# Optimization experiments

Measured on AMD Instinct MI355X. Metric: run time of the kernel, lower is better.

The kernel has to match this reference:

```python
import jax, jax.numpy as jnp
import numpy as np

# Conv-TasNet style TCN: 32 DepthConv1d blocks (8 in, 8 shared, 8 out-branch1, 8 out-branch2)
NUM_BLOCKS = 32
LAYER = 8
DILS = [2 ** (i % LAYER) for i in range(NUM_BLOCKS)]
C_IN, BN, H, OUT, K = 256, 128, 512, 256, 3
B, T = 4, 4000
EPS = 1e-8


def _prelu(x, a):
    return jnp.where(x >= 0, x, a * x)


def _gn(x, g, b):
    # GroupNorm(1, C): normalize over (C, T) per sample. x: [B, C, T]
    m = jnp.mean(x, axis=(1, 2), keepdims=True)
    v = jnp.var(x, axis=(1, 2), keepdims=True)
    return (x - m) * jax.lax.rsqrt(v + EPS) * g[None, :, None] + b[None, :, None]


def _dwconv(x, w, d):
    # depthwise dilated conv, same-length output. x: [B, H, T], w: [H, K]
    return jax.lax.conv_general_dilated(
        x, w[:, None, :], window_strides=(1,), padding=[(d, d)],
        rhs_dilation=(d,), dimension_numbers=('NCH', 'OIH', 'NCH'),
        feature_group_count=w.shape[0])


def _block(x, i, pw_w, pw_b, dw_w, dw_b, res_w, res_b, sk_w, sk_b,
           p1, p2, n1g, n1b, n2g, n2b):
    d = DILS[i]
    y = jnp.einsum('hc,bct->bht', pw_w[i], x) + pw_b[i][None, :, None]
    y = _gn(_prelu(y, p1[i]), n1g[i], n1b[i])
    y = _dwconv(y, dw_w[i], d) + dw_b[i][None, :, None]
    y = _gn(_prelu(y, p2[i]), n2g[i], n2b[i])
    res = jnp.einsum('ch,bht->bct', res_w[i], y) + res_b[i][None, :, None]
    skip = jnp.einsum('ch,bht->bct', sk_w[i], y) + sk_b[i][None, :, None]
    return res, skip


def setup_inputs() -> dict:
    key = jax.random.key(0)
    ks = iter(jax.random.split(key, 64))

    def rn(shape, s=0.05):
        return jax.random.normal(next(ks), shape, dtype=jnp.float32) * s

    L = NUM_BLOCKS
    return {
        'input_r': jax.random.normal(next(ks), (B, C_IN, T), dtype=jnp.float32),
        'ln1_g': jnp.ones((C_IN,), jnp.float32),
        'ln1_b': jnp.zeros((C_IN,), jnp.float32),
        'bn1_w': rn((BN, C_IN)), 'bn1_b': jnp.zeros((BN,), jnp.float32),
        'pw_w': rn((L, H, BN)), 'pw_b': jnp.zeros((L, H), jnp.float32),
        'dw_w': rn((L, H, K)), 'dw_b': jnp.zeros((L, H), jnp.float32),
        'res_w': rn((L, BN, H)), 'res_b': jnp.zeros((L, BN), jnp.float32),
        'sk_w': rn((L, BN, H)), 'sk_b': jnp.zeros((L, BN), jnp.float32),
        'p1': jnp.full((L,), 0.25, jnp.float32), 'p2': jnp.full((L,), 0.25, jnp.float32),
        'n1g': jnp.ones((L, H), jnp.float32), 'n1b': jnp.zeros((L, H), jnp.float32),
        'n2g': jnp.ones((L, H), jnp.float32), 'n2b': jnp.zeros((L, H), jnp.float32),
        'h1_p': jnp.array(0.25, jnp.float32),
        'h1_w': rn((OUT, BN)), 'h1_b': jnp.zeros((OUT,), jnp.float32),
        'h2_p': jnp.array(0.25, jnp.float32),
        'h2_w': rn((OUT, BN)), 'h2_b': jnp.zeros((OUT,), jnp.float32),
    }


def reference(input_r, ln1_g, ln1_b, bn1_w, bn1_b, pw_w, pw_b, dw_w, dw_b,
              res_w, res_b, sk_w, sk_b, p1, p2, n1g, n1b, n2g, n2b,
              h1_p, h1_w, h1_b, h2_p, h2_w, h2_b):
    bp = (pw_w, pw_b, dw_w, dw_b, res_w, res_b, sk_w, sk_b,
          p1, p2, n1g, n1b, n2g, n2b)
    out = _gn(input_r, ln1_g, ln1_b)
    out = jnp.einsum('oc,bct->bot', bn1_w, out) + bn1_b[None, :, None]
    skip_r = jnp.zeros_like(out)
    # TCN_in1: blocks 0..7
    for i in range(0, 8):
        r, s = _block(out, i, *bp)
        out = out + r
        skip_r = skip_r + s
    feature_r = out
    # shared TCN: blocks 8..15
    for i in range(8, 16):
        r, s = _block(out, i, *bp)
        out = out + r
        skip_r = skip_r + s
    o1, o2 = out, out
    sk1, sk2 = skip_r, skip_r
    # TCN_out1: blocks 16..23; TCN_out2: blocks 24..31
    for j in range(8):
        r, s = _block(o1, 16 + j, *bp)
        o1 = o1 + r
        sk1 = sk1 + s
        r, s = _block(o2, 24 + j, *bp)
        o2 = o2 + r
        sk2 = sk2 + s
    out1 = jnp.einsum('oc,bct->bot', h1_w, _prelu(sk1, h1_p)) + h1_b[None, :, None]
    out2 = jnp.einsum('oc,bct->bot', h2_w, _prelu(sk2, h2_p)) + h2_b[None, :, None]
    return out1, out2, feature_r
```

## Files before the change

### kernel.cpp

```cpp
#include <hip/hip_runtime.h>
#include <hip/hip_bf16.h>


#define T_  4000
#define TP_ 4096
#define B_  4
#define YHAL 128
#define YROW 512
#define YSST ((size_t)(TP_ + 2 * YHAL) * YROW)
#define USST ((size_t)TP_ * YROW)
#define NSUB 64
#define SLOTW (NSUB * 8)

typedef __attribute__((ext_vector_type(8))) short  s8v;
typedef __attribute__((ext_vector_type(4))) float  f32x4;
typedef __attribute__((ext_vector_type(4))) unsigned short u16x4;

__device__ __forceinline__ float bf2f(unsigned short u) {
  unsigned int i = ((unsigned int)u) << 16;
  float f; __builtin_memcpy(&f, &i, 4); return f;
}
__device__ __forceinline__ unsigned short f2bf(float f) {
  unsigned int i; __builtin_memcpy(&i, &f, 4);
  unsigned int r = i + 0x7fffu + ((i >> 16) & 1u);
  return (unsigned short)(r >> 16);
}

__device__ __forceinline__ void g2lds16(const void* g, void* l) {
  __builtin_amdgcn_global_load_lds(
      (const __attribute__((address_space(1))) unsigned int*)g,
      (__attribute__((address_space(3))) unsigned int*)l, 16, 0, 0);
}

__device__ __forceinline__ void stats_sum(const float* __restrict__ si, int b,
                                          float& u, float& q) {
  const int lane = threadIdx.x & 63;
  u = si[lane * 8 + b * 2 + 0];
  q = si[lane * 8 + b * 2 + 1];
#pragma unroll
  for (int off = 32; off > 0; off >>= 1) {
    u += __shfl_xor(u, off);
    q += __shfl_xor(q, off);
  }
}

__global__ __launch_bounds__(256) void gn_stats(const float* __restrict__ X,
                                                float* __restrict__ statsOut, int n) {
  const int b = blockIdx.y;
  const float4* xp = (const float4*)(X + (size_t)b * n);
  const int n4 = n >> 2;
  float s1 = 0.f, s2 = 0.f;
  for (int idx = blockIdx.x * 256 + threadIdx.x; idx < n4; idx += gridDim.x * 256) {
    float4 v = xp[idx];
    s1 += v.x + v.y + v.z + v.w;
    s2 += v.x * v.x + v.y * v.y + v.z * v.z + v.w * v.w;
  }
#pragma unroll
  for (int off = 32; off > 0; off >>= 1) {
    s1 += __shfl_xor(s1, off);
    s2 += __shfl_xor(s2, off);
  }
  __shared__ float red[8];
  const int lane = threadIdx.x & 63, wv = threadIdx.x >> 6;
  if (lane == 0) { red[wv] = s1; red[4 + wv] = s2; }
  __syncthreads();
  if (threadIdx.x == 0) {
    float* dst = statsOut + (size_t)(blockIdx.x & (NSUB - 1)) * 8 + b * 2;
    atomicAdd(&dst[0], red[0] + red[1] + red[2] + red[3]);
    atomicAdd(&dst[1], red[4] + red[5] + red[6] + red[7]);
  }
}

__global__ __launch_bounds__(256) void cvt_bf(const float* __restrict__ s,
                                              unsigned short* __restrict__ d, int n) {
  for (int i = blockIdx.x * 256 + threadIdx.x; i < n; i += gridDim.x * 256)
    d[i] = f2bf(s[i]);
}

__global__ __launch_bounds__(256) void fold_rs(
    const float* __restrict__ rw, const float* __restrict__ sw,
    const float* __restrict__ g2a, const float* __restrict__ b2a,
    unsigned short* __restrict__ Wg, float* __restrict__ Ucb,
    float* __restrict__ Vcb) {
  const int row = blockIdx.x;
  const int i = row >> 8, m = row & 255;
  const float* src = (m < 128) ? rw + ((size_t)i * 128 + m) * 512
                               : sw + ((size_t)i * 128 + (m - 128)) * 512;
  const float* g = g2a + (size_t)i * 512;
  const float* bb = b2a + (size_t)i * 512;
  unsigned short* dst = Wg + (size_t)row * 512;
  float u = 0.f, v = 0.f;
  for (int h = threadIdx.x; h < 512; h += 256) {
    float wgt = src[h] * g[h];
    dst[h] = f2bf(wgt);
    u += wgt; v += src[h] * bb[h];
  }
#pragma unroll
  for (int off = 32; off > 0; off >>= 1) {
    u += __shfl_xor(u, off);
    v += __shfl_xor(v, off);
  }
  __shared__ float red[8];
  const int lane = threadIdx.x & 63, wv = threadIdx.x >> 6;
  if (lane == 0) { red[wv] = u; red[4 + wv] = v; }
  __syncthreads();
  if (threadIdx.x == 0) {
    Ucb[row] = red[0] + red[1] + red[2] + red[3];
    Vcb[row] = red[4] + red[5] + red[6] + red[7];
  }
}

__global__ __launch_bounds__(256) void prelu2(const float* __restrict__ S0,
                                              const float* __restrict__ S1,
                                              unsigned short* __restrict__ D,
                                              const float* __restrict__ a0p,
                                              const float* __restrict__ a1p, int n) {
  const float a0 = a0p[0], a1 = a1p[0];
  for (int i = blockIdx.x * 256 + threadIdx.x; i < 2 * n; i += gridDim.x * 256) {
    float v = (i < n) ? S0[i] : S1[i - n];
    float a = (i < n) ? a0 : a1;
    v = v >= 0.f ? v : a * v;
    D[i] = f2bf(v);
  }
}

__global__ __launch_bounds__(256) void tin(const float* __restrict__ X,
                                           unsigned short* __restrict__ Xt,
                                           const float* __restrict__ g,
                                           const float* __restrict__ bt,
                                           const float* __restrict__ sIn, float invN) {
  const int b = blockIdx.z, c0 = blockIdx.y * 64, t0 = blockIdx.x * 64;
  __shared__ float tile[64][65];
  const int tid = threadIdx.x;
  float su, sq;
  stats_sum(sIn, b, su, sq);
  const float mean = su * invN;
  const float rs = rsqrtf(sq * invN - mean * mean + 1e-8f);
  {
    const int cl = tid >> 2, tq = (tid & 3) * 16;
    const float* Xr = X + ((size_t)b * 256 + c0 + cl) * T_;
#pragma unroll
    for (int j = 0; j < 4; ++j) {
      int tt = t0 + tq + j * 4;
      float4 v;
      if (tt + 3 < T_) v = *(const float4*)(Xr + tt);
      else {
        v.x = (tt + 0 < T_) ? Xr[tt + 0] : 0.f;
        v.y = (tt + 1 < T_) ? Xr[tt + 1] : 0.f;
        v.z = (tt + 2 < T_) ? Xr[tt + 2] : 0.f;
        v.w = (tt + 3 < T_) ? Xr[tt + 3] : 0.f;
      }
      tile[cl][tq + j * 4 + 0] = v.x; tile[cl][tq + j * 4 + 1] = v.y;
      tile[cl][tq + j * 4 + 2] = v.z; tile[cl][tq + j * 4 + 3] = v.w;
    }
  }
  __syncthreads();
  {
    const int tl = tid >> 2, cq = (tid & 3) * 16;
    const int t = t0 + tl;
    if (t < T_) {
      unsigned short* dst = Xt + ((size_t)b * TP_ + t) * 256 + c0 + cq;
      s8v u0, u1;
#pragma unroll
      for (int j = 0; j < 16; ++j) {
        int c = c0 + cq + j;
        float sc = rs * g[c];
        float oc = bt[c] - mean * sc;
        unsigned short uu = f2bf(tile[cq + j][tl] * sc + oc);
        if (j < 8) u0[j] = (short)uu; else u1[j - 8] = (short)uu;
      }
      *(s8v*)dst = u0;
      *(s8v*)(dst + 8) = u1;
    }
  }
}

struct MMP {
  const unsigned short *A0, *A1, *B0, *B1;
  const float *bias0, *bias1;
  float *O0a, *O0b, *O1a, *O1b;
  unsigned short *Obf0, *Obf1;
  const float *al0, *al1;
  float *so0, *so1;
  const float *si0, *si1;
  const float *Uc0, *Uc1, *Vc0, *Vc1, *rb0, *rb1, *sb0, *sb1;
  float* feat;
  float* dupO0; unsigned short* dupObf; float* dupO1;
  int K; float invN;
};

template <int EPI, int TN, int FLG>
__global__ __launch_bounds__(256) void mm6(MMP p) {
  constexpr bool PAIR = (FLG & 1) != 0;
  constexpr bool WF   = (FLG & 2) != 0;
  constexpr bool DUPF = (FLG & 4) != 0;
  constexpr int NJ = TN / 32;
  __shared__ unsigned short As[128 * 64];
  __shared__ unsigned short Bs[TN * 64];
  __shared__ float redw[8];
  int b = blockIdx.z; bool br2 = false;
  if constexpr (PAIR) {
    const int h = gridDim.z >> 1;
    if (b >= h) { br2 = true; b -= h; }
  }
  const int K = p.K;
  const unsigned short* A  = br2 ? p.A1 : p.A0;
  const unsigned short* Bm = br2 ? p.B1 : p.B0;
  const int m0 = blockIdx.y * 128;
  const int t0 = blockIdx.x * TN;
  const int tid = threadIdx.x;
  const int lane = tid & 63;
  const int w = tid >> 6;
  const int wm = w >> 1, wn = w & 1;
  const int lt = lane & 15, lg = lane >> 4;
  const unsigned short* Ab = A + (size_t)m0 * K;
  const unsigned short* Bb = Bm + ((size_t)b * TP_ + t0) * K;
  const int srow8 = lane >> 3;
  const int skc   = ((lane & 7) ^ (lane >> 3)) * 8;

  f32x4 acc[4][NJ];
#pragma unroll
  for (int i = 0; i < 4; ++i)
#pragma unroll
    for (int j = 0; j < NJ; ++j) acc[i][j] = (f32x4){0.f, 0.f, 0.f, 0.f};

  for (int k0 = 0; k0 < K; k0 += 64) {
#pragma unroll
    for (int c = 0; c < 4; ++c) {
      const int ch = w * 4 + c;
      g2lds16(Ab + (size_t)(ch * 8 + srow8) * K + k0 + skc, &As[ch * 512]);
    }
#pragma unroll
    for (int c = 0; c < NJ; ++c) {
      const int ch = w * NJ + c;
      g2lds16(Bb + (size_t)(ch * 8 + srow8) * K + k0 + skc, &Bs[ch * 512]);
    }
    __syncthreads();
#pragma unroll
    for (int ks = 0; ks < 2; ++ks) {
      s8v bfr[NJ];
#pragma unroll
      for (int j = 0; j < NJ; ++j) {
        const int R = wn * (TN / 2) + j * 16 + lt;
        bfr[j] = *(const s8v*)&Bs[R * 64 + (((ks * 4 + lg) ^ (R & 7)) * 8)];
      }
#pragma unroll
      for (int i = 0; i < 4; ++i) {
        const int R = wm * 64 + i * 16 + lt;
        s8v af = *(const s8v*)&As[R * 64 + (((ks * 4 + lg) ^ (R & 7)) * 8)];
#pragma unroll
        for (int j = 0; j < NJ; ++j)
          acc[i][j] = __builtin_amdgcn_mfma_f32_16x16x32_bf16(af, bfr[j], acc[i][j], 0, 0, 0);
      }
    }
    __syncthreads();
  }

  if constexpr (EPI == 0) {
    const float* bias = p.bias0;
#pragma unroll
    for (int i = 0; i < 4; ++i) {
      const int mg = m0 + wm * 64 + i * 16 + lg * 4;
      float4 bi = *(const float4*)(bias + mg);
#pragma unroll
      for (int j = 0; j < NJ; ++j) {
        const int t = t0 + wn * (TN / 2) + j * 16 + lt;
        f32x4 v = acc[i][j];
        float nv[4] = {v[0] + bi.x, v[1] + bi.y, v[2] + bi.z, v[3] + bi.w};
        *(float4*)(p.O0a + ((size_t)b * TP_ + t) * 128 + mg) =
            make_float4(nv[0], nv[1], nv[2], nv[3]);
        u16x4 pk;
#pragma unroll
        for (int r = 0; r < 4; ++r) pk[r] = f2bf(nv[r]);
        *(u16x4*)(p.Obf0 + ((size_t)b * TP_ + t) * 128 + mg) = pk;
      }
    }
  } else if constexpr (EPI == 1) {
    const float* bias = br2 ? p.bias1 : p.bias0;
    unsigned short* Obf = (br2 ? p.Obf1 : p.Obf0) + (size_t)b * YSST;
    const float aO = (br2 ? p.al1 : p.al0)[0];
    float* so = br2 ? p.so1 : p.so0;
    float s1 = 0.f, s2 = 0.f;
#pragma unroll
    for (int i = 0; i < 4; ++i) {
      const int mg = m0 + wm * 64 + i * 16 + lg * 4;
      float4 bi = *(const float4*)(bias + mg);
      float bv[4] = {bi.x, bi.y, bi.z, bi.w};
#pragma unroll
      for (int j = 0; j < NJ; ++j) {
        const int t = t0 + wn * (TN / 2) + j * 16 + lt;
        f32x4 v = acc[i][j];
        u16x4 pk;
#pragma unroll
        for (int r = 0; r < 4; ++r) {
          float f = v[r] + bv[r];
          f = f >= 0.f ? f : aO * f;
          pk[r] = f2bf(f);
        }
        *(u16x4*)(Obf + (size_t)t * YROW + mg) = pk;
        if (t < T_) {
#pragma unroll
          for (int r = 0; r < 4; ++r) { float f = bf2f(pk[r]); s1 += f; s2 += f * f; }
        }
      }
    }
#pragma unroll
    for (int off = 32; off > 0; off >>= 1) {
      s1 += __shfl_xor(s1, off);
      s2 += __shfl_xor(s2, off);
    }
    if (lane == 0) { redw[w] = s1; redw[4 + w] = s2; }
    __syncthreads();
    if (tid == 0) {
      float* dst = so + (size_t)(blockIdx.x & (NSUB - 1)) * 8 + b * 2;
      atomicAdd(&dst[0], redw[0] + redw[1] + redw[2] + redw[3]);
      atomicAdd(&dst[1], redw[4] + redw[5] + redw[6] + redw[7]);
    }
  } else if constexpr (EPI == 2) {
    float* O0 = br2 ? p.O0b : p.O0a;
    float* O1 = br2 ? p.O1b : p.O1a;
    unsigned short* Obf = br2 ? p.Obf1 : p.Obf0;
    const float* si = br2 ? p.si1 : p.si0;
    const float* Uc = br2 ? p.Uc1 : p.Uc0;
    const float* Vc = br2 ? p.Vc1 : p.Vc0;
    const float* rb = br2 ? p.rb1 : p.rb0;
    const float* sb = br2 ? p.sb1 : p.sb0;
    float su, sq;
    stats_sum(si, b, su, sq);
    const float mean = su * p.invN;
    const float rsv = rsqrtf(sq * p.invN - mean * mean + 1e-8f);
    const bool isRes = (m0 == 0);
#pragma unroll
    for (int i = 0; i < 4; ++i) {
      const int ml = wm * 64 + i * 16 + lg * 4;
      float cc[4];
#pragma unroll
      for (int r = 0; r < 4; ++r) {
        const int mgG = m0 + ml + r;
        cc[r] = Vc[mgG] - mean * rsv * Uc[mgG] + (isRes ? rb[ml + r] : sb[ml + r]);
      }
#pragma unroll
      for (int j = 0; j < NJ; ++j) {
        const int t = t0 + wn * (TN / 2) + j * 16 + lt;
        f32x4 v = acc[i][j];
        if (isRes) {
          float* ptr = O0 + ((size_t)b * TP_ + t) * 128 + ml;
          float4 old = *(float4*)ptr;
          float nv[4] = {old.x + rsv * v[0] + cc[0], old.y + rsv * v[1] + cc[1],
                         old.z + rsv * v[2] + cc[2], old.w + rsv * v[3] + cc[3]};
          *(float4*)ptr = make_float4(nv[0], nv[1], nv[2], nv[3]);
          u16x4 pk;
#pragma unroll
          for (int r = 0; r < 4; ++r) pk[r] = f2bf(nv[r]);
          *(u16x4*)(Obf + ((size_t)b * TP_ + t) * 128 + ml) = pk;
          if constexpr (DUPF) {
            *(float4*)(p.dupO0 + ((size_t)b * TP_ + t) * 128 + ml) =
                make_float4(nv[0], nv[1], nv[2], nv[3]);
            *(u16x4*)(p.dupObf + ((size_t)b * TP_ + t) * 128 + ml) = pk;
          }
          if constexpr (WF) {
            if (t < T_) {
#pragma unroll
              for (int r = 0; r < 4; ++r)
                p.feat[((size_t)b * 128 + ml + r) * T_ + t] = nv[r];
            }
          }
        } else {
          float* ptr = O1 + ((size_t)b * TP_ + t) * 128 + ml;
          float4 old = *(float4*)ptr;
          float nv[4] = {old.x + rsv * v[0] + cc[0], old.y + rsv * v[1] + cc[1],
                         old.z + rsv * v[2] + cc[2], old.w + rsv * v[3] + cc[3]};
          *(float4*)ptr = make_float4(nv[0], nv[1], nv[2], nv[3]);
          if constexpr (DUPF) {
            *(float4*)(p.dupO1 + ((size_t)b * TP_ + t) * 128 + ml) =
                make_float4(nv[0], nv[1], nv[2], nv[3]);
          }
        }
      }
    }
  } else {
    float* O0 = br2 ? p.O0b : p.O0a;
    const float* bias = br2 ? p.bias1 : p.bias0;
#pragma unroll
    for (int i = 0; i < 4; ++i) {
      const int mg = m0 + wm * 64 + i * 16 + lg * 4;
#pragma unroll
      for (int j = 0; j < NJ; ++j) {
        const int t = t0 + wn * (TN / 2) + j * 16 + lt;
        if (t < T_) {
          f32x4 v = acc[i][j];
#pragma unroll
          for (int r = 0; r < 4; ++r)
            O0[((size_t)b * 256 + mg + r) * T_ + t] = v[r] + bias[mg + r];
        }
      }
    }
  }
}

__global__ __launch_bounds__(256) void dw3(
    const unsigned short* __restrict__ Y, unsigned short* __restrict__ U,
    const float* __restrict__ dww0, const float* __restrict__ dww1,
    const float* __restrict__ dwb0, const float* __restrict__ dwb1,
    const float* __restrict__ g10, const float* __restrict__ g11,
    const float* __restrict__ b10, const float* __restrict__ b11,
    const float* __restrict__ p20, const float* __restrict__ p21,
    const float* __restrict__ sIn0, const float* __restrict__ sIn1, float invN,
    float* __restrict__ sOut0, float* __restrict__ sOut1, int dil, int halfY) {
  const int q = blockIdx.y;
  const bool br2 = q >= halfY;
  const int b = br2 ? q - halfY : q;
  const float* dww = br2 ? dww1 : dww0;
  const float* dwb = br2 ? dwb1 : dwb0;
  const float* g1  = br2 ? g11 : g10;
  const float* b1  = br2 ? b11 : b10;
  const float* p2p = br2 ? p21 : p20;
  const float* sIn = br2 ? sIn1 : sIn0;
  float* sOut      = br2 ? sOut1 : sOut0;
  const int tid = threadIdx.x;
  const int hc = (tid & 63) * 8;
  const int tbase = blockIdx.x * 16 + (tid >> 6) * 4;

  float su, sq2;
  stats_sum(sIn, b, su, sq2);
  const float mean = su * invN;
  const float rs = rsqrtf(sq2 * invN - mean * mean + 1e-8f);
  float sA[8], oA[8], w0[8], w1[8], w2[8], bb[8];
#pragma unroll
  for (int j = 0; j < 8; ++j) {
    sA[j] = rs * g1[hc + j];
    oA[j] = b1[hc + j] - mean * sA[j];
    w0[j] = dww[(hc + j) * 3 + 0];
    w1[j] = dww[(hc + j) * 3 + 1];
    w2[j] = dww[(hc + j) * 3 + 2];
    bb[j] = dwb[hc + j];
  }
  const float alpha = p2p[0];
  const unsigned short* Yb = Y + (size_t)q * YSST;
  unsigned short* Ub = U + (size_t)q * USST;

  s8v xm[4], x0[4], xp[4];
#pragma unroll
  for (int i = 0; i < 4; ++i) {
    const int t = tbase + i;
    xm[i] = *(const s8v*)(Yb + (size_t)(t - dil) * YROW + hc);
    x0[i] = *(const s8v*)(Yb + (size_t)t * YROW + hc);
    xp[i] = *(const s8v*)(Yb + (size_t)(t + dil) * YROW + hc);
  }

  float s1 = 0.f, s2 = 0.f;
#pragma unroll
  for (int i = 0; i < 4; ++i) {
    const int t = tbase + i;
    const bool vm = (t - dil >= 0), vp = (t + dil < T_);
    s8v out;
#pragma unroll
    for (int j = 0; j < 8; ++j) {
      float fm = vm ? (bf2f((unsigned short)xm[i][j]) * sA[j] + oA[j]) : 0.f;
      float f0 = bf2f((unsigned short)x0[i][j]) * sA[j] + oA[j];
      float fp = vp ? (bf2f((unsigned short)xp[i][j]) * sA[j] + oA[j]) : 0.f;
      float v = fmaf(w0[j], fm, fmaf(w1[j], f0, fmaf(w2[j], fp, bb[j])));
      v = v >= 0.f ? v : alpha * v;
      unsigned short u = f2bf(v);
      out[j] = (short)u;
      float f = bf2f(u);
      s1 += f; s2 += f * f;
    }
    *(s8v*)(Ub + (size_t)t * YROW + hc) = out;
  }
#pragma unroll
  for (int off = 32; off > 0; off >>= 1) {
    s1 += __shfl_xor(s1, off);
    s2 += __shfl_xor(s2, off);
  }
  __shared__ float red[8];
  const int lane = tid & 63, wv = tid >> 6;
  if (lane == 0) { red[wv] = s1; red[4 + wv] = s2; }
  __syncthreads();
  if (tid == 0) {
    float* dst = sOut + (size_t)(blockIdx.x & (NSUB - 1)) * 8 + b * 2;
    atomicAdd(&dst[0], red[0] + red[1] + red[2] + red[3]);
    atomicAdd(&dst[1], red[4] + red[5] + red[6] + red[7]);
  }
}

extern "C" void kernel_launch(void* const* d_in, const int* in_sizes, int n_in,
                              void* d_out, int out_size, void* d_ws, size_t ws_size,
                              hipStream_t stream) {
  (void)in_sizes; (void)n_in; (void)out_size; (void)ws_size;
  const float* input = (const float*)d_in[0];
  const float* ln1_g = (const float*)d_in[1];
  const float* ln1_b = (const float*)d_in[2];
  const float* bn1_w = (const float*)d_in[3];
  const float* bn1_b = (const float*)d_in[4];
  const float* pw_w  = (const float*)d_in[5];
  const float* pw_b  = (const float*)d_in[6];
  const float* dw_w  = (const float*)d_in[7];
  const float* dw_b  = (const float*)d_in[8];
  const float* res_w = (const float*)d_in[9];
  const float* res_b = (const float*)d_in[10];
  const float* sk_w  = (const float*)d_in[11];
  const float* sk_b  = (const float*)d_in[12];
  const float* p1    = (const float*)d_in[13];
  const float* p2    = (const float*)d_in[14];
  const float* n1g   = (const float*)d_in[15];
  const float* n1b   = (const float*)d_in[16];
  const float* n2g   = (const float*)d_in[17];
  const float* n2b   = (const float*)d_in[18];
  const float* h1_p  = (const float*)d_in[19];
  const float* h1_w  = (const float*)d_in[20];
  const float* h1_b  = (const float*)d_in[21];
  const float* h2_p  = (const float*)d_in[22];
  const float* h2_w  = (const float*)d_in[23];
  const float* h2_b  = (const float*)d_in[24];

  float* out1 = (float*)d_out;
  float* out2 = out1 + 4096000;
  float* feat = out1 + 8192000;

  char* base = (char*)d_ws;
  float* OUTS  = (float*)base;                  base += (size_t)B_ * TP_ * 128 * 4;
  float* SKIP  = (float*)base;                  base += (size_t)B_ * TP_ * 128 * 4;
  float* OUT2  = (float*)base;                  base += (size_t)B_ * TP_ * 128 * 4;
  float* SKIP2 = (float*)base;                  base += (size_t)B_ * TP_ * 128 * 4;
  unsigned short* OUTbf  = (unsigned short*)base; base += (size_t)B_ * TP_ * 128 * 2;
  unsigned short* OUT2bf = (unsigned short*)base; base += (size_t)B_ * TP_ * 128 * 2;
  unsigned short* Ybuf = (unsigned short*)base; base += (size_t)8 * YSST * 2;
  unsigned short* Ubuf = (unsigned short*)base; base += (size_t)8 * USST * 2;
  unsigned short* Xt   = (unsigned short*)base; base += (size_t)B_ * TP_ * 256 * 2;
  unsigned short* SKbf = (unsigned short*)base; base += (size_t)2 * B_ * TP_ * 128 * 2;
  unsigned short* Wpw  = (unsigned short*)base; base += (size_t)32 * 512 * 128 * 2;
  unsigned short* Wg   = (unsigned short*)base; base += (size_t)32 * 256 * 512 * 2;
  unsigned short* Wbn  = (unsigned short*)base; base += (size_t)128 * 256 * 2;
  unsigned short* Wh1  = (unsigned short*)base; base += (size_t)256 * 128 * 2;
  unsigned short* Wh2  = (unsigned short*)base; base += (size_t)256 * 128 * 2;
  float* UVu   = (float*)base;                  base += (size_t)32 * 256 * 4;
  float* UVv   = (float*)base;                  base += (size_t)32 * 256 * 4;
  float* STATS = (float*)base;

  unsigned short* YbufD = Ybuf + (size_t)YHAL * YROW;
  const int npr = B_ * TP_ * 128;

  hipMemsetAsync(STATS, 0, (size_t)65 * SLOTW * sizeof(float), stream);
  hipMemsetAsync(SKIP, 0, (size_t)B_ * TP_ * 128 * sizeof(float), stream);

  const float invN_in = 1.0f / (256.0f * 4000.0f);
  const float invN_h  = 1.0f / (512.0f * 4000.0f);

  cvt_bf<<<2048, 256, 0, stream>>>(pw_w, Wpw, 32 * 512 * 128);
  cvt_bf<<<128, 256, 0, stream>>>(bn1_w, Wbn, 128 * 256);
  cvt_bf<<<128, 256, 0, stream>>>(h1_w, Wh1, 256 * 128);
  cvt_bf<<<128, 256, 0, stream>>>(h2_w, Wh2, 256 * 128);
  fold_rs<<<32 * 256, 256, 0, stream>>>(res_w, sk_w, n2g, n2b, Wg, UVu, UVv);

  gn_stats<<<dim3(64, B_), 256, 0, stream>>>(input, STATS, 256 * T_);
  tin<<<dim3(63, 4, B_), 256, 0, stream>>>(input, Xt, ln1_g, ln1_b, STATS, invN_in);
  {
    MMP q{}; q.A0 = Wbn; q.B0 = Xt; q.bias0 = bn1_b; q.O0a = OUTS; q.Obf0 = OUTbf;
    q.K = 256;
    mm6<0, 128, 0><<<dim3(32, 1, B_), 256, 0, stream>>>(q);
  }

  auto pw_one = [&](int i) {
    MMP q{}; q.A0 = Wpw + (size_t)i * 512 * 128; q.B0 = OUTbf;
    q.bias0 = pw_b + (size_t)i * 512; q.Obf0 = YbufD; q.al0 = p1 + i;
    q.so0 = STATS + (size_t)(1 + 2 * i) * SLOTW; q.K = 128;
    mm6<1, 128, 0><<<dim3(32, 4, B_), 256, 0, stream>>>(q);
  };
  auto dw_one = [&](int i) {
    float* sA = STATS + (size_t)(1 + 2 * i) * SLOTW;
    float* sB = STATS + (size_t)(2 + 2 * i) * SLOTW;
    dw3<<<dim3(250, B_), 256, 0, stream>>>(
        YbufD, Ubuf, dw_w + (size_t)i * 512 * 3, nullptr,
        dw_b + (size_t)i * 512, nullptr, n1g + (size_t)i * 512, nullptr,
        n1b + (size_t)i * 512, nullptr, p2 + i, nullptr, sA, nullptr, invN_h,
        sB, nullptr, 1 << (i & 7), 99);
  };
  auto rs_one = [&](int i, int flg) {
    MMP q{}; q.A0 = Wg + (size_t)i * 256 * 512; q.B0 = Ubuf;
    q.O0a = OUTS; q.O1a = SKIP; q.Obf0 = OUTbf;
    q.si0 = STATS + (size_t)(2 + 2 * i) * SLOTW; q.invN = invN_h;
    q.Uc0 = UVu + (size_t)i * 256; q.Vc0 = UVv + (size_t)i * 256;
    q.rb0 = res_b + (size_t)i * 128; q.sb0 = sk_b + (size_t)i * 128;
    q.feat = feat; q.dupO0 = OUT2; q.dupObf = OUT2bf; q.dupO1 = SKIP2;
    q.K = 512;
    if (flg == 2)      mm6<2, 64, 2><<<dim3(64, 2, B_), 256, 0, stream>>>(q);
    else if (flg == 4) mm6<2, 64, 4><<<dim3(64, 2, B_), 256, 0, stream>>>(q);
    else               mm6<2, 64, 0><<<dim3(64, 2, B_), 256, 0, stream>>>(q);
  };

  for (int i = 0; i < 16; ++i) {
    pw_one(i);
    dw_one(i);
    rs_one(i, (i == 7) ? 2 : (i == 15) ? 4 : 0);
  }

  for (int j = 0; j < 8; ++j) {
    const int i1 = 16 + j, i2 = 24 + j;
    float* sA1 = STATS + (size_t)(1 + 2 * i1) * SLOTW;
    float* sB1 = STATS + (size_t)(2 + 2 * i1) * SLOTW;
    float* sA2 = STATS + (size_t)(1 + 2 * i2) * SLOTW;
    float* sB2 = STATS + (size_t)(2 + 2 * i2) * SLOTW;
    {
      MMP q{};
      q.A0 = Wpw + (size_t)i1 * 512 * 128; q.A1 = Wpw + (size_t)i2 * 512 * 128;
      q.B0 = OUTbf; q.B1 = OUT2bf;
      q.bias0 = pw_b + (size_t)i1 * 512; q.bias1 = pw_b + (size_t)i2 * 512;
      q.Obf0 = YbufD; q.Obf1 = YbufD + 4 * YSST;
      q.al0 = p1 + i1; q.al1 = p1 + i2;
      q.so0 = sA1; q.so1 = sA2; q.K = 128;
      mm6<1, 128, 1><<<dim3(32, 4, 2 * B_), 256, 0, stream>>>(q);
    }
    dw3<<<dim3(250, 2 * B_), 256, 0, stream>>>(
        YbufD, Ubuf,
        dw_w + (size_t)i1 * 512 * 3, dw_w + (size_t)i2 * 512 * 3,
        dw_b + (size_t)i1 * 512, dw_b + (size_t)i2 * 512,
        n1g + (size_t)i1 * 512, n1g + (size_t)i2 * 512,
        n1b + (size_t)i1 * 512, n1b + (size_t)i2 * 512,
        p2 + i1, p2 + i2, sA1, sA2, invN_h, sB1, sB2, 1 << (j & 7), B_);
    {
      MMP q{};
      q.A0 = Wg + (size_t)i1 * 256 * 512; q.A1 = Wg + (size_t)i2 * 256 * 512;
      q.B0 = Ubuf; q.B1 = Ubuf + 4 * USST;
      q.O0a = OUTS; q.O0b = OUT2; q.O1a = SKIP; q.O1b = SKIP2;
      q.Obf0 = OUTbf; q.Obf1 = OUT2bf;
      q.si0 = sB1; q.si1 = sB2; q.invN = invN_h;
      q.Uc0 = UVu + (size_t)i1 * 256; q.Uc1 = UVu + (size_t)i2 * 256;
      q.Vc0 = UVv + (size_t)i1 * 256; q.Vc1 = UVv + (size_t)i2 * 256;
      q.rb0 = res_b + (size_t)i1 * 128; q.rb1 = res_b + (size_t)i2 * 128;
      q.sb0 = sk_b + (size_t)i1 * 128; q.sb1 = sk_b + (size_t)i2 * 128;
      q.K = 512;
      mm6<2, 128, 1><<<dim3(32, 2, 2 * B_), 256, 0, stream>>>(q);
    }
  }

  prelu2<<<2048, 256, 0, stream>>>(SKIP, SKIP2, SKbf, h1_p, h2_p, npr);
  {
    MMP q{};
    q.A0 = Wh1; q.A1 = Wh2;
    q.B0 = SKbf; q.B1 = SKbf + npr;
    q.bias0 = h1_b; q.bias1 = h2_b;
    q.O0a = out1; q.O0b = out2; q.K = 128;
    mm6<3, 128, 1><<<dim3(32, 2, 2 * B_), 256, 0, stream>>>(q);
  }
}
```

Baseline: 1.269 ms.

## Fuse next block's pointwise conv into residual/skip GEMM epilogue for first 16 blocks

Adds a kernel rsp that runs the residual/skip GEMM, writes the updated bf16 output tile into shared memory, and then in the res-half blocks runs the next block's 128->512 pointwise conv with bias, PReLU, bf16 store and GroupNorm stat accumulation. This removes one kernel launch per block and the re-read of the fresh output from global memory for blocks 1-15. In exchange, the pointwise GEMM is done by only half the grid (blockIdx.y==0) with A operands loaded straight from global memory and a large accumulator array, which raises register pressure and leaves the load uneven across workgroups.

```diff
diff --git a/kernel.cpp b/kernel.cpp
--- a/kernel.cpp
+++ b/kernel.cpp
@@ -394,6 +394,191 @@
             O0[((size_t)b * 256 + mg + r) * T_ + t] = v[r] + bias[mg + r];
         }
       }
+    }
+  }
+}
+
+template <int FLG>
+__global__ __launch_bounds__(256) void rsp(MMP p) {
+  constexpr bool WF = (FLG & 2) != 0;
+  constexpr int TN = 64;
+  constexpr int NJ = 2;
+  __shared__ unsigned short As[128 * 64];
+  __shared__ unsigned short Bs[TN * 64];
+  __shared__ float redw[8];
+  const int b = blockIdx.z;
+  const int m0 = blockIdx.y * 128;
+  const int t0 = blockIdx.x * TN;
+  const int tid = threadIdx.x;
+  const int lane = tid & 63;
+  const int w = tid >> 6;
+  const int wm = w >> 1, wn = w & 1;
+  const int lt = lane & 15, lg = lane >> 4;
+  const int K = 512;
+  const unsigned short* Ab = p.A0 + (size_t)m0 * K;
+  const unsigned short* Bb = p.B0 + ((size_t)b * TP_ + t0) * K;
+  const int srow8 = lane >> 3;
+  const int skc   = ((lane & 7) ^ (lane >> 3)) * 8;
+
+  f32x4 acc[4][NJ];
+#pragma unroll
+  for (int i = 0; i < 4; ++i)
+#pragma unroll
+    for (int j = 0; j < NJ; ++j) acc[i][j] = (f32x4){0.f, 0.f, 0.f, 0.f};
+
+  for (int k0 = 0; k0 < K; k0 += 64) {
+#pragma unroll
+    for (int c = 0; c < 4; ++c) {
+      const int ch = w * 4 + c;
+      g2lds16(Ab + (size_t)(ch * 8 + srow8) * K + k0 + skc, &As[ch * 512]);
+    }
+#pragma unroll
+    for (int c = 0; c < NJ; ++c) {
+      const int ch = w * NJ + c;
+      g2lds16(Bb + (size_t)(ch * 8 + srow8) * K + k0 + skc, &Bs[ch * 512]);
+    }
+    __syncthreads();
+#pragma unroll
+    for (int ks = 0; ks < 2; ++ks) {
+      s8v bfr[NJ];
+#pragma unroll
+      for (int j = 0; j < NJ; ++j) {
+        const int R = wn * (TN / 2) + j * 16 + lt;
+        bfr[j] = *(const s8v*)&Bs[R * 64 + (((ks * 4 + lg) ^ (R & 7)) * 8)];
+      }
+#pragma unroll
+      for (int i = 0; i < 4; ++i) {
+        const int R = wm * 64 + i * 16 + lt;
+        s8v af = *(const s8v*)&As[R * 64 + (((ks * 4 + lg) ^ (R & 7)) * 8)];
+#pragma unroll
+        for (int j = 0; j < NJ; ++j)
+          acc[i][j] = __builtin_amdgcn_mfma_f32_16x16x32_bf16(af, bfr[j], acc[i][j], 0, 0, 0);
+      }
+    }
+    __syncthreads();
+  }
+
+  {
+    float su, sq;
+    stats_sum(p.si0, b, su, sq);
+    const float mean = su * p.invN;
+    const float rsv = rsqrtf(sq * p.invN - mean * mean + 1e-8f);
+    const bool isRes = (m0 == 0);
+#pragma unroll
+    for (int i = 0; i < 4; ++i) {
+      const int ml = wm * 64 + i * 16 + lg * 4;
+      float cc[4];
+#pragma unroll
+      for (int r = 0; r < 4; ++r) {
+        const int mgG = m0 + ml + r;
+        cc[r] = p.Vc0[mgG] - mean * rsv * p.Uc0[mgG] +
+                (isRes ? p.rb0[ml + r] : p.sb0[ml + r]);
+      }
+#pragma unroll
+      for (int j = 0; j < NJ; ++j) {
+        const int t = t0 + wn * 32 + j * 16 + lt;
+        f32x4 v = acc[i][j];
+        if (isRes) {
+          float* ptr = p.O0a + ((size_t)b * TP_ + t) * 128 + ml;
+          float4 old = *(float4*)ptr;
+          float nv[4] = {old.x + rsv * v[0] + cc[0], old.y + rsv * v[1] + cc[1],
+                         old.z + rsv * v[2] + cc[2], old.w + rsv * v[3] + cc[3]};
+          *(float4*)ptr = make_float4(nv[0], nv[1], nv[2], nv[3]);
+          u16x4 pk;
+#pragma unroll
+          for (int r = 0; r < 4; ++r) pk[r] = f2bf(nv[r]);
+          *(u16x4*)(p.Obf0 + ((size_t)b * TP_ + t) * 128 + ml) = pk;
+          const int tl = wn * 32 + j * 16 + lt;
+          const int c4 = wm * 16 + i * 4 + lg;
+          *(u16x4*)&As[tl * 128 + (c4 ^ (2 * (tl & 7))) * 4] = pk;
+          if constexpr (WF) {
+            if (t < T_) {
+#pragma unroll
+              for (int r = 0; r < 4; ++r)
+                p.feat[((size_t)b * 128 + ml + r) * T_ + t] = nv[r];
+            }
+          }
+        } else {
+          float* ptr = p.O1a + ((size_t)b * TP_ + t) * 128 + ml;
+          float4 old = *(float4*)ptr;
+          *(float4*)ptr = make_float4(old.x + rsv * v[0] + cc[0],
+                                      old.y + rsv * v[1] + cc[1],
+                                      old.z + rsv * v[2] + cc[2],
+                                      old.w + rsv * v[3] + cc[3]);
+        }
+      }
+    }
+  }
+
+  if (blockIdx.y == 0) {
+    __syncthreads();
+    const unsigned short* A2 = p.A1;
+    f32x4 acc2[8][4];
+#pragma unroll
+    for (int i2 = 0; i2 < 8; ++i2)
+#pragma unroll
+      for (int j2 = 0; j2 < 4; ++j2) acc2[i2][j2] = (f32x4){0.f, 0.f, 0.f, 0.f};
+#pragma unroll
+    for (int kk = 0; kk < 2; ++kk) {
+#pragma unroll
+      for (int ks = 0; ks < 2; ++ks) {
+        s8v bv[4];
+#pragma unroll
+        for (int j2 = 0; j2 < 4; ++j2) {
+          const int R2 = j2 * 16 + lt;
+          const int q = kk * 8 + ks * 4 + lg;
+          bv[j2] = *(const s8v*)&As[R2 * 128 + (q ^ (R2 & 7)) * 8];
+        }
+        s8v av[8];
+#pragma unroll
+        for (int i2 = 0; i2 < 8; ++i2) {
+          const int R = w * 128 + i2 * 16 + lt;
+          av[i2] = *(const s8v*)(A2 + (size_t)R * 128 + kk * 64 + ks * 32 + lg * 8);
+        }
+#pragma unroll
+        for (int i2 = 0; i2 < 8; ++i2)
+#pragma unroll
+          for (int j2 = 0; j2 < 4; ++j2)
+            acc2[i2][j2] = __builtin_amdgcn_mfma_f32_16x16x32_bf16(av[i2], bv[j2], acc2[i2][j2], 0, 0, 0);
+      }
+    }
+    const float aO = p.al1[0];
+    unsigned short* Yd = p.Obf1 + (size_t)b * YSST;
+    float s1 = 0.f, s2 = 0.f;
+#pragma unroll
+    for (int i2 = 0; i2 < 8; ++i2) {
+      const int mg = w * 128 + i2 * 16 + lg * 4;
+      float4 bi = *(const float4*)(p.bias1 + mg);
+      float bvv[4] = {bi.x, bi.y, bi.z, bi.w};
+#pragma unroll
+      for (int j2 = 0; j2 < 4; ++j2) {
+        const int t = t0 + j2 * 16 + lt;
+        f32x4 v = acc2[i2][j2];
+        u16x4 pk;
+#pragma unroll
+        for (int r = 0; r < 4; ++r) {
+          float f = v[r] + bvv[r];
+          f = f >= 0.f ? f : aO * f;
+          pk[r] = f2bf(f);
+        }
+        *(u16x4*)(Yd + (size_t)t * YROW + mg) = pk;
+        if (t < T_) {
+#pragma unroll
+          for (int r = 0; r < 4; ++r) { float f = bf2f(pk[r]); s1 += f; s2 += f * f; }
+        }
+      }
+    }
+#pragma unroll
+    for (int off = 32; off > 0; off >>= 1) {
+      s1 += __shfl_xor(s1, off);
+      s2 += __shfl_xor(s2, off);
+    }
+    if (lane == 0) { redw[w] = s1; redw[4 + w] = s2; }
+    __syncthreads();
+    if (tid == 0) {
+      float* dst = p.so1 + (size_t)(blockIdx.x & (NSUB - 1)) * 8 + b * 2;
+      atomicAdd(&dst[0], redw[0] + redw[1] + redw[2] + redw[3]);
+      atomicAdd(&dst[1], redw[4] + redw[5] + redw[6] + redw[7]);
     }
   }
 }
@@ -584,16 +769,31 @@
     q.rb0 = res_b + (size_t)i * 128; q.sb0 = sk_b + (size_t)i * 128;
     q.feat = feat; q.dupO0 = OUT2; q.dupObf = OUT2bf; q.dupO1 = SKIP2;
     q.K = 512;
-    if (flg == 2)      mm6<2, 64, 2><<<dim3(64, 2, B_), 256, 0, stream>>>(q);
-    else if (flg == 4) mm6<2, 64, 4><<<dim3(64, 2, B_), 256, 0, stream>>>(q);
-    else               mm6<2, 64, 0><<<dim3(64, 2, B_), 256, 0, stream>>>(q);
+    if (flg == 4) mm6<2, 64, 4><<<dim3(64, 2, B_), 256, 0, stream>>>(q);
+    else          mm6<2, 64, 0><<<dim3(64, 2, B_), 256, 0, stream>>>(q);
   };
 
-  for (int i = 0; i < 16; ++i) {
-    pw_one(i);
-    dw_one(i);
-    rs_one(i, (i == 7) ? 2 : (i == 15) ? 4 : 0);
-  }
+  pw_one(0);
+  dw_one(0);
+  for (int i = 0; i < 15; ++i) {
+    MMP q{};
+    q.A0 = Wg + (size_t)i * 256 * 512; q.B0 = Ubuf;
+    q.O0a = OUTS; q.O1a = SKIP; q.Obf0 = OUTbf;
+    q.si0 = STATS + (size_t)(2 + 2 * i) * SLOTW; q.invN = invN_h;
+    q.Uc0 = UVu + (size_t)i * 256; q.Vc0 = UVv + (size_t)i * 256;
+    q.rb0 = res_b + (size_t)i * 128; q.sb0 = sk_b + (size_t)i * 128;
+    q.feat = feat;
+    q.A1 = Wpw + (size_t)(i + 1) * 512 * 128;
+    q.bias1 = pw_b + (size_t)(i + 1) * 512;
+    q.al1 = p1 + (i + 1);
+    q.so1 = STATS + (size_t)(1 + 2 * (i + 1)) * SLOTW;
+    q.Obf1 = YbufD;
+    q.K = 512;
+    if (i == 7) rsp<2><<<dim3(64, 2, B_), 256, 0, stream>>>(q);
+    else        rsp<0><<<dim3(64, 2, B_), 256, 0, stream>>>(q);
+    dw_one(i + 1);
+  }
+  rs_one(15, 4);
 
   for (int j = 0; j < 8; ++j) {
     const int i1 = 16 + j, i2 = 24 + j;
```

Result: slower. 1.310 ms (+3.3%).
